# Optimization experiments

Measured on AMD Instinct MI355X. Metric: run time of the kernel, lower is better.

Reference implementation:

```python
import jax, jax.numpy as jnp
import numpy as np

N_NODES = 50000
N_EDGES = 1600000
IN_CH = 128
OUT_CH = 128
MAX_NORM = 1.0


def setup_inputs() -> dict:
    key = jax.random.key(0)
    k1, k2, k3, k4 = jax.random.split(key, 4)
    x = jax.random.normal(k1, (N_NODES, IN_CH), dtype=jnp.float32)
    edge_index = jax.random.randint(k2, (2, N_EDGES), 0, N_NODES, dtype=jnp.int64)
    # GCNConv lin: weight [out, in] (kaiming-ish init), bias [out] zeros-ish
    W = jax.random.normal(k3, (OUT_CH, IN_CH), dtype=jnp.float32) * (1.0 / np.sqrt(IN_CH))
    b = jax.random.normal(k4, (OUT_CH,), dtype=jnp.float32) * 0.01
    return {"x": x, "edge_index": edge_index, "W": W, "b": b}


def _renorm_cols(W, max_norm):
    # torch.renorm(W, p=2, dim=1, maxnorm): each slice along dim 1 (column of [out,in])
    # is rescaled so its L2 norm <= max_norm.
    norms = jnp.sqrt(jnp.sum(W * W, axis=0, keepdims=True))  # [1, in]
    scale = jnp.where(norms > max_norm, max_norm / norms, 1.0)
    return W * scale


def reference(x, edge_index, W, b):
    N = x.shape[0]
    Wn = _renorm_cols(W, MAX_NORM)
    # Linear transform first (as PyG GCNConv does): h = x @ W^T
    h = jnp.einsum('ni,oi->no', x, Wn)  # [N, out]

    # Add self loops
    row = jnp.concatenate([edge_index[0], jnp.arange(N, dtype=edge_index.dtype)])
    col = jnp.concatenate([edge_index[1], jnp.arange(N, dtype=edge_index.dtype)])

    # Symmetric normalization: deg over destination (col), edge weights = 1
    ones = jnp.ones(row.shape[0], dtype=h.dtype)
    deg = jax.ops.segment_sum(ones, col, num_segments=N)
    deg_inv_sqrt = jnp.where(deg > 0, jax.lax.rsqrt(deg), 0.0)
    norm = deg_inv_sqrt[row] * deg_inv_sqrt[col]  # [E+N]

    # Gather source features, scale, scatter-add to destinations
    msgs = h[row] * norm[:, None]  # [E+N, out]
    out = jax.ops.segment_sum(msgs, col, num_segments=N)
    return out + b
```

## Files before the change

### kernel.cpp

```cpp
#include <hip/hip_runtime.h>

#define N_NODES 50000
#define N_EDGES 1600000
#define CH 128
#define NB 196
#define CHUNK_E 2048
#define NCHUNK 782
#define GEMMB 782
#define CAP 12288

#define WS_CURSOR  0
#define WS_ROWPTR  1024
#define WS_DINV    201728
#define WS_SCL     401728
#define WS_SRC     601728
#define WS_Q8      7001728
#define WS_BINS    13401728

typedef __bf16 bf16x8 __attribute__((ext_vector_type(8)));
typedef float f32x4 __attribute__((ext_vector_type(4)));

__device__ __forceinline__ unsigned int pack_bf16(float a, float b) {
    unsigned int ua = __builtin_bit_cast(unsigned int, a);
    unsigned int ub = __builtin_bit_cast(unsigned int, b);
    ua = (ua + 0x7FFFu + ((ua >> 16) & 1u)) >> 16;
    ub = (ub + 0x7FFFu + ((ub >> 16) & 1u)) >> 16;
    return ua | (ub << 16);
}

__device__ __forceinline__ void acc4(unsigned int v, float sc, float* a) {
    a[0] = fmaf((float)(v & 0xFFu), sc, a[0]);
    a[1] = fmaf((float)((v >> 8) & 0xFFu), sc, a[1]);
    a[2] = fmaf((float)((v >> 16) & 0xFFu), sc, a[2]);
    a[3] = fmaf((float)(v >> 24), sc, a[3]);
}

__global__ __launch_bounds__(256) void k_fused(const float* __restrict__ x,
                                               const float* __restrict__ W,
                                               const int* __restrict__ eidx,
                                               int* __restrict__ cursor,
                                               unsigned int* __restrict__ bins,
                                               unsigned int* __restrict__ q8,
                                               float* __restrict__ scl) {
    __shared__ uint4 SMEM[3072];
    __shared__ float s_scale[128];
    __shared__ float s_part[256];
    __shared__ int s_st;
    int t = threadIdx.x;

    if (blockIdx.x < NCHUNK) {
        int c = blockIdx.x;
        int* lc    = (int*)SMEM;
        int* lbase = (int*)SMEM + 256;
        unsigned int* stash = (unsigned int*)SMEM + 512;
        lc[t] = 0;
        if (t < 64) {
            int v = eidx[2 * t + 1];
            unsigned long long m = __ballot(v == 0);
            if (t == 0) s_st = (m == ~0ull) ? 2 : 1;
        }
        __syncthreads();
        int st = s_st;
        long base = (long)c * CHUNK_E;
        #pragma unroll
        for (int i = 0; i < 4; ++i) {
            long e0 = base + (long)(i * 256 + t) * 2;
            unsigned int u0 = 0xFFFFFFFFu, u1 = 0xFFFFFFFFu;
            if (e0 < N_EDGES) {
                unsigned int r0, r1, c0, c1;
                if (st == 2) {
                    uint4 rw = *(const uint4*)&eidx[2 * e0];
                    uint4 cw = *(const uint4*)&eidx[2 * (N_EDGES + e0)];
                    r0 = rw.x; r1 = rw.z; c0 = cw.x; c1 = cw.z;
                } else {
                    uint2 rw = *(const uint2*)&eidx[e0];
                    uint2 cw = *(const uint2*)&eidx[N_EDGES + e0];
                    r0 = rw.x; r1 = rw.y; c0 = cw.x; c1 = cw.y;
                }
                u0 = r0 | (c0 << 16);
                u1 = r1 | (c1 << 16);
                atomicAdd(&lc[c0 >> 8], 1);
                atomicAdd(&lc[c1 >> 8], 1);
            }
            stash[i * 512 + 2 * t]     = u0;
            stash[i * 512 + 2 * t + 1] = u1;
        }
        __syncthreads();
        if (t < NB && lc[t] > 0) lbase[t] = atomicAdd(&cursor[t], lc[t]);
        __syncthreads();
        #pragma unroll
        for (int i = 0; i < 8; ++i) {
            unsigned int u = stash[i * 256 + t];
            if (u != 0xFFFFFFFFu) {
                int bb = u >> 24;
                int pos = atomicAdd(&lbase[bb], 1);
                bins[(size_t)bb * CAP + pos] = (u & 0xFFFFu) | (((u >> 16) & 0xFFu) << 16);
            }
        }
        return;
    }

    uint4* xs = SMEM;
    uint4* wsl = SMEM + 1024;
    float* scratch = (float*)SMEM;
    int base = (blockIdx.x - NCHUNK) * 64;
    {
        int ct = t & 127, oh = (t >> 7) * 64;
        float s = 0.f;
        #pragma unroll 8
        for (int o = 0; o < 64; ++o) {
            float w = W[(size_t)(oh + o) * CH + ct];
            s += w * w;
        }
        s_part[t] = s;
        __syncthreads();
        if (t < 128) {
            float tot = s_part[t] + s_part[t + 128];
            s_scale[t] = (tot > 1.0f) ? rsqrtf(tot) : 1.0f;
        }
    }
    #pragma unroll
    for (int it = 0; it < 4; ++it) {
        int idx = it * 256 + t;
        int r = idx >> 4, c16 = idx & 15;
        int n = base + r;
        float4 v0 = make_float4(0.f, 0.f, 0.f, 0.f), v1 = v0;
        if (n < N_NODES) {
            v0 = *(const float4*)&x[(size_t)n * CH + c16 * 8];
            v1 = *(const float4*)&x[(size_t)n * CH + c16 * 8 + 4];
        }
        uint4 p;
        p.x = pack_bf16(v0.x, v0.y); p.y = pack_bf16(v0.z, v0.w);
        p.z = pack_bf16(v1.x, v1.y); p.w = pack_bf16(v1.z, v1.w);
        xs[r * 16 + (c16 ^ (r & 7))] = p;
    }
    __syncthreads();
    #pragma unroll
    for (int it = 0; it < 8; ++it) {
        int idx = it * 256 + t;
        int o = idx >> 4, c16 = idx & 15;
        float4 v0 = *(const float4*)&W[(size_t)o * CH + c16 * 8];
        float4 v1 = *(const float4*)&W[(size_t)o * CH + c16 * 8 + 4];
        int k0 = c16 * 8;
        v0.x *= s_scale[k0];     v0.y *= s_scale[k0 + 1];
        v0.z *= s_scale[k0 + 2]; v0.w *= s_scale[k0 + 3];
        v1.x *= s_scale[k0 + 4]; v1.y *= s_scale[k0 + 5];
        v1.z *= s_scale[k0 + 6]; v1.w *= s_scale[k0 + 7];
        uint4 p;
        p.x = pack_bf16(v0.x, v0.y); p.y = pack_bf16(v0.z, v0.w);
        p.z = pack_bf16(v1.x, v1.y); p.w = pack_bf16(v1.z, v1.w);
        wsl[o * 16 + (c16 ^ (o & 7))] = p;
    }
    __syncthreads();
    int w = t >> 6, l = t & 63;
    int lrow = w * 16 + (l & 15);
    int hi = l >> 4;
    bf16x8 a[4];
    #pragma unroll
    for (int ks = 0; ks < 4; ++ks) {
        int c16 = ks * 4 + hi;
        a[ks] = __builtin_bit_cast(bf16x8, xs[lrow * 16 + (c16 ^ (lrow & 7))]);
    }
    float vals[8][4];
    #pragma unroll
    for (int tc = 0; tc < 8; ++tc) {
        int col = tc * 16 + (l & 15);
        f32x4 acc = {0.f, 0.f, 0.f, 0.f};
        #pragma unroll
        for (int ks = 0; ks < 4; ++ks) {
            int c16 = ks * 4 + hi;
            bf16x8 bf = __builtin_bit_cast(bf16x8, wsl[col * 16 + (c16 ^ (col & 7))]);
            acc = __builtin_amdgcn_mfma_f32_16x16x32_bf16(a[ks], bf, acc, 0, 0, 0);
        }
        #pragma unroll
        for (int r = 0; r < 4; ++r) vals[tc][r] = acc[r];
    }
    __syncthreads();
    #pragma unroll
    for (int tc = 0; tc < 8; ++tc) {
        int col = tc * 16 + (l & 15);
        #pragma unroll
        for (int r = 0; r < 4; ++r) {
            int rl = w * 16 + hi * 4 + r;
            scratch[rl * 132 + col] = vals[tc][r];
        }
    }
    __syncthreads();
    int rl = t >> 2, q = t & 3;
    const float4* rp = (const float4*)&scratch[rl * 132 + q * 32];
    float4 f[8];
    float m = 0.f;
    #pragma unroll
    for (int k = 0; k < 8; ++k) {
        f[k] = rp[k];
        m = fmaxf(m, fmaxf(fmaxf(fabsf(f[k].x), fabsf(f[k].y)),
                           fmaxf(fabsf(f[k].z), fabsf(f[k].w))));
    }
    m = fmaxf(m, __shfl_xor(m, 1));
    m = fmaxf(m, __shfl_xor(m, 2));
    float sc = m * (1.0f / 127.0f);
    float inv = (m > 0.f) ? (127.0f / m) : 0.f;
    int n = base + rl;
    if (n < N_NODES) {
        unsigned int u[8];
        #pragma unroll
        for (int k = 0; k < 8; ++k) {
            int b0 = __float2int_rn(f[k].x * inv) + 128;
            int b1 = __float2int_rn(f[k].y * inv) + 128;
            int b2 = __float2int_rn(f[k].z * inv) + 128;
            int b3 = __float2int_rn(f[k].w * inv) + 128;
            u[k] = (unsigned int)b0 | ((unsigned int)b1 << 8) |
                   ((unsigned int)b2 << 16) | ((unsigned int)b3 << 24);
        }
        uint4* qp = (uint4*)&q8[(size_t)n * 32 + q * 8];
        qp[0] = make_uint4(u[0], u[1], u[2], u[3]);
        qp[1] = make_uint4(u[4], u[5], u[6], u[7]);
        if (q == 0) scl[n] = sc;
    }
}

__global__ __launch_bounds__(256) void k_sort(const unsigned int* __restrict__ bins,
                                              const int* __restrict__ cursor,
                                              int* __restrict__ rowptr,
                                              float* __restrict__ dinv,
                                              float* __restrict__ scl,
                                              int* __restrict__ src) {
    __shared__ int shA[256], shB[256], shC[256];
    __shared__ int s_g0, s_sz;
    int t = threadIdx.x, b = blockIdx.x;
    int v = (t < NB) ? cursor[t] : 0;
    shC[t] = v;
    __syncthreads();
    for (int off = 1; off < 256; off <<= 1) {
        int u = (t >= off) ? shC[t - off] : 0;
        __syncthreads();
        shC[t] += u;
        __syncthreads();
    }
    if (t == b) { s_g0 = shC[t] - v; s_sz = v; }
    __syncthreads();
    int g0 = s_g0, sz = s_sz;
    const unsigned int* reg = bins + (size_t)b * CAP;
    shA[t] = 0;
    __syncthreads();
    for (int i = t; i < sz; i += 256) {
        unsigned int p = reg[i];
        atomicAdd(&shA[(p >> 16) & 255], 1);
    }
    __syncthreads();
    int d = shA[t];
    shC[t] = d;
    __syncthreads();
    for (int off = 1; off < 256; off <<= 1) {
        int u = (t >= off) ? shC[t - off] : 0;
        __syncthreads();
        shC[t] += u;
        __syncthreads();
    }
    int local_rp = g0 + shC[t] - d;
    int n = (b << 8) + t;
    if (n < N_NODES) {
        rowptr[n] = local_rp;
        float dv = rsqrtf((float)(d + 1));
        dinv[n] = dv;
        scl[n] *= dv;
    }
    if (b == NB - 1 && t == 0) rowptr[N_NODES] = N_EDGES;
    shB[t] = local_rp;
    __syncthreads();
    for (int i = t; i < sz; i += 256) {
        unsigned int p = reg[i];
        int pos = atomicAdd(&shB[(p >> 16) & 255], 1);
        src[pos] = (int)(p & 0xFFFFu);
    }
}

__global__ __launch_bounds__(256) void k_gather(const int* __restrict__ rowptr,
                                                const int* __restrict__ src,
                                                const uint4* __restrict__ q8v,
                                                const float* __restrict__ scl,
                                                const float* __restrict__ dinv,
                                                const float* __restrict__ b,
                                                float* __restrict__ out) {
    int t = threadIdx.x;
    int wid = t >> 6, l = t & 63;
    int g = l >> 3;
    int c8 = l & 7;
    int n = blockIdx.x * 4 + wid;
    if (n >= N_NODES) return;
    int j0 = rowptr[n], j1 = rowptr[n + 1];
    float acc[16];
    #pragma unroll
    for (int i = 0; i < 16; ++i) acc[i] = 0.f;
    float asum = 0.f;
    for (int jj = j0; jj < j1; jj += 16) {
        int eA = jj + g, eB = jj + 8 + g;
        bool vA = eA < j1, vB = eB < j1;
        int sA = vA ? src[eA] : 0;
        int sB = vB ? src[eB] : 0;
        float scA = vA ? scl[sA] : 0.f;
        float scB = vB ? scl[sB] : 0.f;
        uint4 qA = q8v[(size_t)sA * 8 + c8];
        uint4 qB = q8v[(size_t)sB * 8 + c8];
        asum += scA + scB;
        acc4(qA.x, scA, &acc[0]);  acc4(qA.y, scA, &acc[4]);
        acc4(qA.z, scA, &acc[8]);  acc4(qA.w, scA, &acc[12]);
        acc4(qB.x, scB, &acc[0]);  acc4(qB.y, scB, &acc[4]);
        acc4(qB.z, scB, &acc[8]);  acc4(qB.w, scB, &acc[12]);
    }
    #pragma unroll
    for (int i = 0; i < 16; ++i) {
        acc[i] += __shfl_xor(acc[i], 8);
        acc[i] += __shfl_xor(acc[i], 16);
        acc[i] += __shfl_xor(acc[i], 32);
    }
    asum += __shfl_xor(asum, 8);
    asum += __shfl_xor(asum, 16);
    asum += __shfl_xor(asum, 32);
    if (l < 8) {
        float di = dinv[n];
        float scn = scl[n];
        uint4 sv = q8v[(size_t)n * 8 + c8];
        float bias128 = 128.0f * asum;
        const float4* bp = (const float4*)&b[c8 * 16];
        float4* op = (float4*)&out[(size_t)n * CH + c8 * 16];
        unsigned int svw[4] = {sv.x, sv.y, sv.z, sv.w};
        #pragma unroll
        for (int w4 = 0; w4 < 4; ++w4) {
            unsigned int v = svw[w4];
            float4 bv = bp[w4];
            float4 o;
            o.x = (acc[w4 * 4 + 0] - bias128 + ((float)(v & 0xFFu) - 128.f) * scn) * di + bv.x;
            o.y = (acc[w4 * 4 + 1] - bias128 + ((float)((v >> 8) & 0xFFu) - 128.f) * scn) * di + bv.y;
            o.z = (acc[w4 * 4 + 2] - bias128 + ((float)((v >> 16) & 0xFFu) - 128.f) * scn) * di + bv.z;
            o.w = (acc[w4 * 4 + 3] - bias128 + ((float)(v >> 24) - 128.f) * scn) * di + bv.w;
            op[w4] = o;
        }
    }
}

extern "C" void kernel_launch(void* const* d_in, const int* in_sizes, int n_in,
                              void* d_out, int out_size, void* d_ws, size_t ws_size,
                              hipStream_t stream) {
    const float* x = (const float*)d_in[0];
    const int* eidx = (const int*)d_in[1];
    const float* W = (const float*)d_in[2];
    const float* b = (const float*)d_in[3];
    float* out = (float*)d_out;

    char* ws = (char*)d_ws;
    int*   cursor        = (int*)(ws + WS_CURSOR);
    int*   rowptr        = (int*)(ws + WS_ROWPTR);
    float* dinv          = (float*)(ws + WS_DINV);
    float* sclp          = (float*)(ws + WS_SCL);
    int*   srcarr        = (int*)(ws + WS_SRC);
    unsigned int* q8     = (unsigned int*)(ws + WS_Q8);
    unsigned int* bins   = (unsigned int*)(ws + WS_BINS);

    hipMemsetAsync(cursor, 0, NB * sizeof(int), stream);
    k_fused<<<NCHUNK + GEMMB, 256, 0, stream>>>(x, W, eidx, cursor, bins, q8, sclp);
    k_sort<<<NB, 256, 0, stream>>>(bins, cursor, rowptr, dinv, sclp, srcarr);
    k_gather<<<(N_NODES + 3) / 4, 256, 0, stream>>>(rowptr, srcarr, (const uint4*)q8,
                                                    sclp, dinv, b, out);
}
```

Measured before the change: 112.1 us.

## Precompute renormalized bf16 weights once and shrink GEMM shared memory

Adds a single-block prep kernel that computes the column renorm and packs W to bf16 once. GEMM blocks then read their B fragments straight from global memory, which should be L2-resident, instead of every block recomputing norms and staging W in LDS. The epilogue is split into two 32-row passes so the shared buffer drops from about 48KB to about 17KB, which raises occupancy for both the binning and GEMM blocks. The cost is an extra serialized launch with a slow single-block prep, plus uncoalesced-ish global fragment loads in the MFMA loop.

```diff
diff --git a/kernel.cpp b/kernel.cpp
--- a/kernel.cpp
+++ b/kernel.cpp
@@ -10,12 +10,13 @@
 #define CAP 12288
 
 #define WS_CURSOR  0
-#define WS_ROWPTR  1024
-#define WS_DINV    201728
-#define WS_SCL     401728
-#define WS_SRC     601728
-#define WS_Q8      7001728
-#define WS_BINS    13401728
+#define WS_WBF     1024
+#define WS_ROWPTR  33792
+#define WS_DINV    234496
+#define WS_SCL     435200
+#define WS_SRC     635904
+#define WS_Q8      7035904
+#define WS_BINS    13435904
 
 typedef __bf16 bf16x8 __attribute__((ext_vector_type(8)));
 typedef float f32x4 __attribute__((ext_vector_type(4)));
@@ -35,16 +36,28 @@
     a[3] = fmaf((float)(v >> 24), sc, a[3]);
 }
 
+__global__ void k_prep(const float* __restrict__ W, unsigned int* __restrict__ Wbf) {
+    __shared__ float s_scale[128];
+    int t = threadIdx.x;
+    float s = 0.f;
+    for (int o = 0; o < CH; ++o) { float w = W[o * CH + t]; s += w * w; }
+    s_scale[t] = (s > 1.0f) ? rsqrtf(s) : 1.0f;
+    __syncthreads();
+    for (int k16 = 0; k16 < 64; ++k16) {
+        float a = W[t * CH + 2 * k16]     * s_scale[2 * k16];
+        float b = W[t * CH + 2 * k16 + 1] * s_scale[2 * k16 + 1];
+        Wbf[t * 64 + k16] = pack_bf16(a, b);
+    }
+}
+
 __global__ __launch_bounds__(256) void k_fused(const float* __restrict__ x,
-                                               const float* __restrict__ W,
+                                               const unsigned int* __restrict__ Wbf,
                                                const int* __restrict__ eidx,
                                                int* __restrict__ cursor,
                                                unsigned int* __restrict__ bins,
                                                unsigned int* __restrict__ q8,
                                                float* __restrict__ scl) {
-    __shared__ uint4 SMEM[3072];
-    __shared__ float s_scale[128];
-    __shared__ float s_part[256];
+    __shared__ uint4 SMEM[1056];
     __shared__ int s_st;
     int t = threadIdx.x;
 
@@ -101,24 +114,8 @@
     }
 
     uint4* xs = SMEM;
-    uint4* wsl = SMEM + 1024;
     float* scratch = (float*)SMEM;
     int base = (blockIdx.x - NCHUNK) * 64;
-    {
-        int ct = t & 127, oh = (t >> 7) * 64;
-        float s = 0.f;
-        #pragma unroll 8
-        for (int o = 0; o < 64; ++o) {
-            float w = W[(size_t)(oh + o) * CH + ct];
-            s += w * w;
-        }
-        s_part[t] = s;
-        __syncthreads();
-        if (t < 128) {
-            float tot = s_part[t] + s_part[t + 128];
-            s_scale[t] = (tot > 1.0f) ? rsqrtf(tot) : 1.0f;
-        }
-    }
     #pragma unroll
     for (int it = 0; it < 4; ++it) {
         int idx = it * 256 + t;
@@ -135,23 +132,6 @@
         xs[r * 16 + (c16 ^ (r & 7))] = p;
     }
     __syncthreads();
-    #pragma unroll
-    for (int it = 0; it < 8; ++it) {
-        int idx = it * 256 + t;
-        int o = idx >> 4, c16 = idx & 15;
-        float4 v0 = *(const float4*)&W[(size_t)o * CH + c16 * 8];
-        float4 v1 = *(const float4*)&W[(size_t)o * CH + c16 * 8 + 4];
-        int k0 = c16 * 8;
-        v0.x *= s_scale[k0];     v0.y *= s_scale[k0 + 1];
-        v0.z *= s_scale[k0 + 2]; v0.w *= s_scale[k0 + 3];
-        v1.x *= s_scale[k0 + 4]; v1.y *= s_scale[k0 + 5];
-        v1.z *= s_scale[k0 + 6]; v1.w *= s_scale[k0 + 7];
-        uint4 p;
-        p.x = pack_bf16(v0.x, v0.y); p.y = pack_bf16(v0.z, v0.w);
-        p.z = pack_bf16(v1.x, v1.y); p.w = pack_bf16(v1.z, v1.w);
-        wsl[o * 16 + (c16 ^ (o & 7))] = p;
-    }
-    __syncthreads();
     int w = t >> 6, l = t & 63;
     int lrow = w * 16 + (l & 15);
     int hi = l >> 4;
@@ -161,61 +141,66 @@
         int c16 = ks * 4 + hi;
         a[ks] = __builtin_bit_cast(bf16x8, xs[lrow * 16 + (c16 ^ (lrow & 7))]);
     }
+    int colb = l & 15;
     float vals[8][4];
     #pragma unroll
     for (int tc = 0; tc < 8; ++tc) {
-        int col = tc * 16 + (l & 15);
+        int col = tc * 16 + colb;
         f32x4 acc = {0.f, 0.f, 0.f, 0.f};
         #pragma unroll
         for (int ks = 0; ks < 4; ++ks) {
             int c16 = ks * 4 + hi;
-            bf16x8 bf = __builtin_bit_cast(bf16x8, wsl[col * 16 + (c16 ^ (col & 7))]);
-            acc = __builtin_amdgcn_mfma_f32_16x16x32_bf16(a[ks], bf, acc, 0, 0, 0);
+            uint4 wf = *(const uint4*)&Wbf[col * 64 + c16 * 4];
+            acc = __builtin_amdgcn_mfma_f32_16x16x32_bf16(a[ks],
+                      __builtin_bit_cast(bf16x8, wf), acc, 0, 0, 0);
         }
         #pragma unroll
         for (int r = 0; r < 4; ++r) vals[tc][r] = acc[r];
     }
     __syncthreads();
     #pragma unroll
-    for (int tc = 0; tc < 8; ++tc) {
-        int col = tc * 16 + (l & 15);
-        #pragma unroll
-        for (int r = 0; r < 4; ++r) {
-            int rl = w * 16 + hi * 4 + r;
-            scratch[rl * 132 + col] = vals[tc][r];
-        }
-    }
-    __syncthreads();
-    int rl = t >> 2, q = t & 3;
-    const float4* rp = (const float4*)&scratch[rl * 132 + q * 32];
-    float4 f[8];
-    float m = 0.f;
-    #pragma unroll
-    for (int k = 0; k < 8; ++k) {
-        f[k] = rp[k];
-        m = fmaxf(m, fmaxf(fmaxf(fabsf(f[k].x), fabsf(f[k].y)),
-                           fmaxf(fabsf(f[k].z), fabsf(f[k].w))));
-    }
-    m = fmaxf(m, __shfl_xor(m, 1));
-    m = fmaxf(m, __shfl_xor(m, 2));
-    float sc = m * (1.0f / 127.0f);
-    float inv = (m > 0.f) ? (127.0f / m) : 0.f;
-    int n = base + rl;
-    if (n < N_NODES) {
-        unsigned int u[8];
-        #pragma unroll
-        for (int k = 0; k < 8; ++k) {
-            int b0 = __float2int_rn(f[k].x * inv) + 128;
-            int b1 = __float2int_rn(f[k].y * inv) + 128;
-            int b2 = __float2int_rn(f[k].z * inv) + 128;
-            int b3 = __float2int_rn(f[k].w * inv) + 128;
-            u[k] = (unsigned int)b0 | ((unsigned int)b1 << 8) |
-                   ((unsigned int)b2 << 16) | ((unsigned int)b3 << 24);
-        }
-        uint4* qp = (uint4*)&q8[(size_t)n * 32 + q * 8];
-        qp[0] = make_uint4(u[0], u[1], u[2], u[3]);
-        qp[1] = make_uint4(u[4], u[5], u[6], u[7]);
-        if (q == 0) scl[n] = sc;
+    for (int pass = 0; pass < 2; ++pass) {
+        if ((w >> 1) == pass) {
+            int rbase = (w & 1) * 16 + hi * 4;
+            #pragma unroll
+            for (int tc = 0; tc < 8; ++tc) {
+                #pragma unroll
+                for (int r = 0; r < 4; ++r)
+                    scratch[(rbase + r) * 132 + tc * 16 + colb] = vals[tc][r];
+            }
+        }
+        __syncthreads();
+        int row32 = t >> 3, piece = t & 7;
+        const float4* rp = (const float4*)&scratch[row32 * 132 + piece * 16];
+        float4 f[4];
+        float m = 0.f;
+        #pragma unroll
+        for (int k = 0; k < 4; ++k) {
+            f[k] = rp[k];
+            m = fmaxf(m, fmaxf(fmaxf(fabsf(f[k].x), fabsf(f[k].y)),
+                               fmaxf(fabsf(f[k].z), fabsf(f[k].w))));
+        }
+        m = fmaxf(m, __shfl_xor(m, 1));
+        m = fmaxf(m, __shfl_xor(m, 2));
+        m = fmaxf(m, __shfl_xor(m, 4));
+        float sc = m * (1.0f / 127.0f);
+        float inv = (m > 0.f) ? (127.0f / m) : 0.f;
+        int n = base + pass * 32 + row32;
+        if (n < N_NODES) {
+            unsigned int uw[4];
+            #pragma unroll
+            for (int k = 0; k < 4; ++k) {
+                int b0 = __float2int_rn(f[k].x * inv) + 128;
+                int b1 = __float2int_rn(f[k].y * inv) + 128;
+                int b2 = __float2int_rn(f[k].z * inv) + 128;
+                int b3 = __float2int_rn(f[k].w * inv) + 128;
+                uw[k] = (unsigned int)b0 | ((unsigned int)b1 << 8) |
+                        ((unsigned int)b2 << 16) | ((unsigned int)b3 << 24);
+            }
+            ((uint4*)&q8[(size_t)n * 32])[piece] = make_uint4(uw[0], uw[1], uw[2], uw[3]);
+            if (piece == 0) scl[n] = sc;
+        }
+        __syncthreads();
     }
 }
 
@@ -350,6 +335,7 @@
 
     char* ws = (char*)d_ws;
     int*   cursor        = (int*)(ws + WS_CURSOR);
+    unsigned int* Wbf    = (unsigned int*)(ws + WS_WBF);
     int*   rowptr        = (int*)(ws + WS_ROWPTR);
     float* dinv          = (float*)(ws + WS_DINV);
     float* sclp          = (float*)(ws + WS_SCL);
@@ -358,7 +344,8 @@
     unsigned int* bins   = (unsigned int*)(ws + WS_BINS);
 
     hipMemsetAsync(cursor, 0, NB * sizeof(int), stream);
-    k_fused<<<NCHUNK + GEMMB, 256, 0, stream>>>(x, W, eidx, cursor, bins, q8, sclp);
+    k_prep<<<1, 128, 0, stream>>>(W, Wbf);
+    k_fused<<<NCHUNK + GEMMB, 256, 0, stream>>>(x, Wbf, eidx, cursor, bins, q8, sclp);
     k_sort<<<NB, 256, 0, stream>>>(bins, cursor, rowptr, dinv, sclp, srcarr);
     k_gather<<<(N_NODES + 3) / 4, 256, 0, stream>>>(rowptr, srcarr, (const uint4*)q8,
                                                     sclp, dinv, b, out);
```

Result: slower. 123.9 us (+10.5%).
